# Performance work log

Measured on AMD Instinct MI355X. Metric: run time of the kernel, lower is better.

The kernel has to match this reference:

```python
import jax, jax.numpy as jnp
import numpy as np

N_NODES = 50000
IN, H, OUT = 128, 256, 128  # in_channels, hidden_channels, out_channels
E, PE = 640000, 500000
EPS = 1e-5


def setup_inputs() -> dict:
    key = jax.random.key(0)
    ks = jax.random.split(key, 12)
    def rn(k, shape, s=0.05):
        return jax.random.normal(k, shape, jnp.float32) * s
    return {
        "x": jax.random.normal(ks[0], (N_NODES, IN), jnp.float32),
        "edge_index": jax.random.randint(ks[1], (2, E), 0, N_NODES, jnp.int32),
        "pred_edge_index": jax.random.randint(ks[2], (2, PE), 0, N_NODES, jnp.int32),
        # SAGEConv 1: out = mean_neighbors @ W_l^T + x @ W_r^T + b (PyG default, root_weight=True)
        "W1l": rn(ks[3], (H, IN)), "W1r": rn(ks[4], (H, IN)), "b1": jnp.zeros((H,), jnp.float32),
        "bn1_g": jnp.ones((H,), jnp.float32), "bn1_b": jnp.zeros((H,), jnp.float32),
        "bn1_m": jnp.zeros((H,), jnp.float32), "bn1_v": jnp.ones((H,), jnp.float32),
        # SAGEConv 2
        "W2l": rn(ks[5], (OUT, H)), "W2r": rn(ks[6], (OUT, H)), "b2": jnp.zeros((OUT,), jnp.float32),
        # LinkPredictor MLP
        "pW1": rn(ks[7], (H, 2 * OUT)), "pb1": jnp.zeros((H,), jnp.float32),
        "pbn1_g": jnp.ones((H,), jnp.float32), "pbn1_b": jnp.zeros((H,), jnp.float32),
        "pbn1_m": jnp.zeros((H,), jnp.float32), "pbn1_v": jnp.ones((H,), jnp.float32),
        "pW2": rn(ks[8], (H // 2, H)), "pb2": jnp.zeros((H // 2,), jnp.float32),
        "pbn2_g": jnp.ones((H // 2,), jnp.float32), "pbn2_b": jnp.zeros((H // 2,), jnp.float32),
        "pbn2_m": jnp.zeros((H // 2,), jnp.float32), "pbn2_v": jnp.ones((H // 2,), jnp.float32),
        "pW3": rn(ks[9], (1, H // 2)), "pb3": jnp.zeros((1,), jnp.float32),
    }


def _bn(x, g, b, m, v):
    # BatchNorm1d in eval mode (running stats)
    return (x - m) * jax.lax.rsqrt(v + EPS) * g + b


def _sage(x, src, dst, Wl, Wr, b):
    # mean aggregation of source features onto targets (gather-scatter)
    agg = jax.ops.segment_sum(x[src], dst, num_segments=N_NODES)
    cnt = jax.ops.segment_sum(jnp.ones(src.shape, x.dtype), dst, num_segments=N_NODES)
    mean = agg / jnp.maximum(cnt, 1.0)[:, None]
    return mean @ Wl.T + x @ Wr.T + b


def reference(x, edge_index, pred_edge_index, W1l, W1r, b1, bn1_g, bn1_b, bn1_m, bn1_v,
              W2l, W2r, b2, pW1, pb1, pbn1_g, pbn1_b, pbn1_m, pbn1_v,
              pW2, pb2, pbn2_g, pbn2_b, pbn2_m, pbn2_v, pW3, pb3):
    src, dst = edge_index[0], edge_index[1]
    # encoder (dropout is identity in eval mode)
    h = _sage(x, src, dst, W1l, W1r, b1)
    h = jax.nn.relu(_bn(h, bn1_g, bn1_b, bn1_m, bn1_v))
    z = _sage(h, src, dst, W2l, W2r, b2)  # [N_NODES, OUT]
    # decoder: gather endpoint embeddings and run MLP
    q = jnp.concatenate([z[pred_edge_index[0]], z[pred_edge_index[1]]], axis=-1)  # [PE, 2*OUT]
    q = jax.nn.relu(_bn(q @ pW1.T + pb1, pbn1_g, pbn1_b, pbn1_m, pbn1_v))
    q = jax.nn.relu(_bn(q @ pW2.T + pb2, pbn2_g, pbn2_b, pbn2_m, pbn2_v))
    return (q @ pW3.T + pb3).squeeze(-1)  # [PE]
```

## Files before the change

### kernel.cpp

```cpp
#include <hip/hip_runtime.h>
#include <hip/hip_bf16.h>

#define NN   50000
#define NE   640000
#define NPE  500000
#define FEPS 1e-5f

typedef __attribute__((ext_vector_type(8))) short          bf16x8;
typedef __attribute__((ext_vector_type(8))) unsigned short u16x8;
typedef __attribute__((ext_vector_type(4))) float          f32x4;

__device__ inline float b2f(unsigned short u) {
    union { unsigned int i; float f; } c; c.i = (unsigned int)u << 16; return c.f;
}
__device__ inline unsigned short f2b(float f) {
    __hip_bfloat16 h = __float2bfloat16(f);
    return *reinterpret_cast<unsigned short*>(&h);
}

__global__ __launch_bounds__(256) void k_init(
    int4* __restrict__ zdst,
    const float* __restrict__ x, unsigned short* __restrict__ xbf,
    const float* __restrict__ W1l, const float* __restrict__ W1r,
    const float* __restrict__ W2l, const float* __restrict__ W2r,
    const float* __restrict__ pW1, const float* __restrict__ pW2,
    unsigned short* __restrict__ wdst) {
    int b = blockIdx.x, t = threadIdx.x;
    if (b < 98) {
        int i = b * 256 + t;
        if (i < 25088) zdst[i] = make_int4(0, 0, 0, 0);
        return;
    }
    const float* src;
    size_t off;
    if (b < 3223) {
        int i = (b - 98) * 256 + t;
        if (i >= 800000) return;
        const float4* p = (const float4*)x + 2 * (size_t)i;
        float4 a = p[0], c = p[1];
        u16x8 o;
        o[0]=f2b(a.x); o[1]=f2b(a.y); o[2]=f2b(a.z); o[3]=f2b(a.w);
        o[4]=f2b(c.x); o[5]=f2b(c.y); o[6]=f2b(c.z); o[7]=f2b(c.w);
        *((u16x8*)xbf + i) = o;
        return;
    }
    int i = (b - 3223) * 256 + t;
    if (i >= 28672) return;
    if      (i < 4096)  { src = W1l; off = i; }
    else if (i < 8192)  { src = W1r; off = i - 4096; }
    else if (i < 12288) { src = W2l; off = i - 8192; }
    else if (i < 16384) { src = W2r; off = i - 12288; }
    else if (i < 24576) { src = pW1; off = i - 16384; }
    else                { src = pW2; off = i - 24576; }
    const float4* p = (const float4*)src + 2 * off;
    float4 a = p[0], c = p[1];
    u16x8 o;
    o[0]=f2b(a.x); o[1]=f2b(a.y); o[2]=f2b(a.z); o[3]=f2b(a.w);
    o[4]=f2b(c.x); o[5]=f2b(c.y); o[6]=f2b(c.z); o[7]=f2b(c.w);
    *((u16x8*)wdst + i) = o;
}

__global__ void k_hist(const int* __restrict__ key, int* __restrict__ cnt, int n) {
    int e = blockIdx.x * blockDim.x + threadIdx.x;
    if (e < n) atomicAdd(&cnt[key[e]], 1);
}

__global__ void k_scan1(const int* __restrict__ cnt, int* __restrict__ part) {
    int t = threadIdx.x, lane = t & 63, w = t >> 6;
    int i = blockIdx.x * 256 + t;
    int v = (i < NN) ? cnt[i] : 0;
#pragma unroll
    for (int d = 1; d < 64; d <<= 1) v += __shfl_xor(v, d, 64);
    __shared__ int ws[4];
    if (lane == 0) ws[w] = v;
    __syncthreads();
    if (t == 0) part[blockIdx.x] = ws[0] + ws[1] + ws[2] + ws[3];
}

__global__ void k_scan2(int* __restrict__ part) {
    int t = threadIdx.x, lane = t & 63, w = t >> 6;
    int v = (t < 196) ? part[t] : 0;
    int s = v;
#pragma unroll
    for (int d = 1; d < 64; d <<= 1) { int u = __shfl_up(s, d, 64); if (lane >= d) s += u; }
    __shared__ int ws[4];
    if (lane == 63) ws[w] = s;
    __syncthreads();
    if (t == 0) { int a = 0; for (int k = 0; k < 4; ++k) { int tmp = ws[k]; ws[k] = a; a += tmp; } }
    __syncthreads();
    if (t < 196) part[t] = ws[w] + s - v;
}

__global__ void k_scan3(const int* __restrict__ cnt, const int* __restrict__ part,
                        int* __restrict__ rowptr) {
    int t = threadIdx.x, lane = t & 63, w = t >> 6;
    int i = blockIdx.x * 256 + t;
    int v = (i < NN) ? cnt[i] : 0;
    int s = v;
#pragma unroll
    for (int d = 1; d < 64; d <<= 1) { int u = __shfl_up(s, d, 64); if (lane >= d) s += u; }
    __shared__ int ws[4];
    if (lane == 63) ws[w] = s;
    __syncthreads();
    if (t == 0) { int a = 0; for (int k = 0; k < 4; ++k) { int tmp = ws[k]; ws[k] = a; a += tmp; } }
    __syncthreads();
    if (i <= NN) rowptr[i] = part[blockIdx.x] + ws[w] + s - v;
}

__global__ void k_fill(const int* __restrict__ src, const int* __restrict__ dst,
                       const int* __restrict__ rowptr, int* __restrict__ cursor,
                       int* __restrict__ col) {
    int e = blockIdx.x * blockDim.x + threadIdx.x;
    if (e >= NE) return;
    int d = dst[e];
    int slot = atomicAdd(&cursor[d], 1);
    col[rowptr[d] + slot] = src[e];
}

__global__ __launch_bounds__(256) void k_mean(const unsigned short* __restrict__ feat,
                                              const int* __restrict__ rowptr,
                                              const int* __restrict__ col,
                                              unsigned short* __restrict__ outm) {
    int node = blockIdx.x * 4 + (threadIdx.x >> 6);
    int lane = threadIdx.x & 63;
    int g = lane >> 4, li = lane & 15;
    if (node >= NN) return;
    int beg = rowptr[node], end = rowptr[node + 1];
    float acc[8];
#pragma unroll
    for (int k = 0; k < 8; ++k) acc[k] = 0.f;
    int j = beg;
    for (; j + 8 <= end; j += 8) {
        int s0 = col[j + g], s1 = col[j + 4 + g];
        u16x8 v0 = *(const u16x8*)(feat + (size_t)s0 * 128 + li * 8);
        u16x8 v1 = *(const u16x8*)(feat + (size_t)s1 * 128 + li * 8);
#pragma unroll
        for (int k = 0; k < 8; ++k)
            acc[k] += b2f((unsigned short)v0[k]) + b2f((unsigned short)v1[k]);
    }
    for (; j < end; j += 4) {
        int idx = j + g;
        bool ok = idx < end;
        int s = ok ? col[idx] : col[beg];
        u16x8 v = *(const u16x8*)(feat + (size_t)s * 128 + li * 8);
        if (ok) {
#pragma unroll
            for (int k = 0; k < 8; ++k) acc[k] += b2f((unsigned short)v[k]);
        }
    }
#pragma unroll
    for (int k = 0; k < 8; ++k) {
        acc[k] += __shfl_xor(acc[k], 16, 64);
        acc[k] += __shfl_xor(acc[k], 32, 64);
    }
    if (g == 0) {
        float inv = 1.f / fmaxf((float)(end - beg), 1.f);
        u16x8 o;
#pragma unroll
        for (int k = 0; k < 8; ++k) o[k] = f2b(acc[k] * inv);
        *(u16x8*)(outm + (size_t)node * 128 + li * 8) = o;
    }
}

__global__ __launch_bounds__(256) void k_sage12(
    const unsigned short* __restrict__ mean, const unsigned short* __restrict__ self,
    const unsigned short* __restrict__ Wl, const unsigned short* __restrict__ Wr,
    const float* __restrict__ b, const float* __restrict__ bg, const float* __restrict__ bb,
    const float* __restrict__ bm, const float* __restrict__ bv,
    const unsigned short* __restrict__ W2l, const unsigned short* __restrict__ W2r,
    const float* __restrict__ b2,
    unsigned short* __restrict__ Y, unsigned short* __restrict__ S) {
    __shared__ unsigned short AB[64 * 256];
    unsigned short* ms = AB;
    unsigned short* xs = AB + 64 * 128;
    int t = threadIdx.x;
    int n0 = blockIdx.x * 64;
    for (int j = 0; j < 4; ++j) {
        int idx = t + j * 256;
        int row = idx >> 4, c16 = idx & 15;
        int node = n0 + row;
        u16x8 v = {0,0,0,0,0,0,0,0}, v2 = {0,0,0,0,0,0,0,0};
        if (node < NN) {
            v  = *(const u16x8*)(mean + (size_t)node * 128 + c16 * 8);
            v2 = *(const u16x8*)(self + (size_t)node * 128 + c16 * 8);
        }
        int byte = row * 256 + ((c16 * 16) ^ ((row & 7) << 4));
        *(u16x8*)((char*)ms + byte) = v;
        *(u16x8*)((char*)xs + byte) = v2;
    }
    __syncthreads();
    int w = t >> 6, l = t & 63, lr = l & 15, lh = l >> 4;
    f32x4 acc[4][4];
#pragma unroll
    for (int mi = 0; mi < 4; ++mi)
#pragma unroll
        for (int ni = 0; ni < 4; ++ni) { acc[mi][ni][0]=0; acc[mi][ni][1]=0; acc[mi][ni][2]=0; acc[mi][ni][3]=0; }
#pragma unroll
    for (int half = 0; half < 2; ++half) {
        const unsigned short* A = half ? xs : ms;
        const unsigned short* W = half ? Wr : Wl;
#pragma unroll
        for (int ks = 0; ks < 4; ++ks) {
            int k0 = ks * 32;
            bf16x8 a[4], wf[4];
#pragma unroll
            for (int mi = 0; mi < 4; ++mi) {
                int row = mi * 16 + lr;
                int byte = row * 256 + ((k0 * 2 + lh * 16) ^ ((row & 7) << 4));
                a[mi] = *(const bf16x8*)((const char*)A + byte);
            }
#pragma unroll
            for (int ni = 0; ni < 4; ++ni) {
                int wrow = w * 64 + ni * 16 + lr;
                wf[ni] = *(const bf16x8*)(W + (size_t)wrow * 128 + k0 + lh * 8);
            }
#pragma unroll
            for (int mi = 0; mi < 4; ++mi)
#pragma unroll
                for (int ni = 0; ni < 4; ++ni)
                    acc[mi][ni] = __builtin_amdgcn_mfma_f32_16x16x32_bf16(a[mi], wf[ni], acc[mi][ni], 0, 0, 0);
        }
    }
    __syncthreads();
#pragma unroll
    for (int ni = 0; ni < 4; ++ni) {
        int ch = w * 64 + ni * 16 + lr;
        float sc = bg[ch] * rsqrtf(bv[ch] + FEPS);
        float sh = bb[ch] - bm[ch] * sc;
        float bias = b[ch];
#pragma unroll
        for (int mi = 0; mi < 4; ++mi)
#pragma unroll
            for (int r = 0; r < 4; ++r) {
                int row = mi * 16 + lh * 4 + r;
                float vv = fmaxf((acc[mi][ni][r] + bias) * sc + sh, 0.f);
                int byte = row * 512 + ((ch * 2) ^ ((row & 7) << 4));
                *(unsigned short*)((char*)AB + byte) = f2b(vv);
            }
    }
    __syncthreads();
    f32x4 aY[4][2], aS[4][2];
#pragma unroll
    for (int mi = 0; mi < 4; ++mi)
#pragma unroll
        for (int ni = 0; ni < 2; ++ni) {
            aY[mi][ni][0]=0; aY[mi][ni][1]=0; aY[mi][ni][2]=0; aY[mi][ni][3]=0;
            aS[mi][ni][0]=0; aS[mi][ni][1]=0; aS[mi][ni][2]=0; aS[mi][ni][3]=0;
        }
#pragma unroll
    for (int ks = 0; ks < 8; ++ks) {
        int k0 = ks * 32;
        bf16x8 a[4], wl[2], wr[2];
#pragma unroll
        for (int mi = 0; mi < 4; ++mi) {
            int row = mi * 16 + lr;
            int byte = row * 512 + ((k0 * 2 + lh * 16) ^ ((row & 7) << 4));
            a[mi] = *(const bf16x8*)((const char*)AB + byte);
        }
#pragma unroll
        for (int ni = 0; ni < 2; ++ni) {
            int wrow = w * 32 + ni * 16 + lr;
            wl[ni] = *(const bf16x8*)(W2l + (size_t)wrow * 256 + k0 + lh * 8);
            wr[ni] = *(const bf16x8*)(W2r + (size_t)wrow * 256 + k0 + lh * 8);
        }
#pragma unroll
        for (int mi = 0; mi < 4; ++mi)
#pragma unroll
            for (int ni = 0; ni < 2; ++ni) {
                aY[mi][ni] = __builtin_amdgcn_mfma_f32_16x16x32_bf16(a[mi], wl[ni], aY[mi][ni], 0, 0, 0);
                aS[mi][ni] = __builtin_amdgcn_mfma_f32_16x16x32_bf16(a[mi], wr[ni], aS[mi][ni], 0, 0, 0);
            }
    }
#pragma unroll
    for (int ni = 0; ni < 2; ++ni) {
        int ch = w * 32 + ni * 16 + lr;
        float bias = b2[ch];
#pragma unroll
        for (int mi = 0; mi < 4; ++mi)
#pragma unroll
            for (int r = 0; r < 4; ++r) {
                int node = n0 + mi * 16 + lh * 4 + r;
                if (node < NN) {
                    Y[(size_t)node * 128 + ch] = f2b(aY[mi][ni][r]);
                    S[(size_t)node * 128 + ch] = f2b(aS[mi][ni][r] + bias);
                }
            }
    }
}

__global__ __launch_bounds__(256) void k_prep(
    const unsigned short* __restrict__ S,
    const unsigned short* __restrict__ mY,
    const unsigned short* __restrict__ W1,
    const float* __restrict__ b1, const float* __restrict__ g1,
    const float* __restrict__ be1, const float* __restrict__ m1, const float* __restrict__ v1,
    unsigned short* __restrict__ Pa, unsigned short* __restrict__ Pb) {
    __shared__ unsigned short zs[64 * 128];
    int t = threadIdx.x;
    int n0 = blockIdx.x * 64;
    for (int j = 0; j < 4; ++j) {
        int idx = t + j * 256;
        int row = idx >> 4, c16 = idx & 15;
        int node = n0 + row;
        u16x8 o = {0,0,0,0,0,0,0,0};
        if (node < NN) {
            u16x8 sv = *(const u16x8*)(S  + (size_t)node * 128 + c16 * 8);
            u16x8 mv = *(const u16x8*)(mY + (size_t)node * 128 + c16 * 8);
#pragma unroll
            for (int jj = 0; jj < 8; ++jj)
                o[jj] = f2b(b2f((unsigned short)sv[jj]) + b2f((unsigned short)mv[jj]));
        }
        int byte = row * 256 + ((c16 * 16) ^ ((row & 7) << 4));
        *(u16x8*)((char*)zs + byte) = o;
    }
    __syncthreads();
    int w = t >> 6, l = t & 63, lr = l & 15, lh = l >> 4;
#pragma unroll
    for (int side = 0; side < 2; ++side) {
        f32x4 acc[4][4];
#pragma unroll
        for (int mi = 0; mi < 4; ++mi)
#pragma unroll
            for (int ni = 0; ni < 4; ++ni) { acc[mi][ni][0]=0; acc[mi][ni][1]=0; acc[mi][ni][2]=0; acc[mi][ni][3]=0; }
#pragma unroll
        for (int ks = 0; ks < 4; ++ks) {
            int k0 = ks * 32;
            bf16x8 a[4], wf[4];
#pragma unroll
            for (int mi = 0; mi < 4; ++mi) {
                int row = mi * 16 + lr;
                int byte = row * 256 + ((k0 * 2 + lh * 16) ^ ((row & 7) << 4));
                a[mi] = *(const bf16x8*)((const char*)zs + byte);
            }
#pragma unroll
            for (int ni = 0; ni < 4; ++ni) {
                int ch = w * 64 + ni * 16 + lr;
                wf[ni] = *(const bf16x8*)(W1 + (size_t)ch * 256 + side * 128 + k0 + lh * 8);
            }
#pragma unroll
            for (int mi = 0; mi < 4; ++mi)
#pragma unroll
                for (int ni = 0; ni < 4; ++ni)
                    acc[mi][ni] = __builtin_amdgcn_mfma_f32_16x16x32_bf16(a[mi], wf[ni], acc[mi][ni], 0, 0, 0);
        }
        unsigned short* P = side ? Pb : Pa;
#pragma unroll
        for (int ni = 0; ni < 4; ++ni) {
            int ch = w * 64 + ni * 16 + lr;
            float sc = g1[ch] * rsqrtf(v1[ch] + FEPS);
            float add = side ? 0.f : ((b1[ch] - m1[ch]) * sc + be1[ch]);
#pragma unroll
            for (int mi = 0; mi < 4; ++mi)
#pragma unroll
                for (int r = 0; r < 4; ++r) {
                    int node = n0 + mi * 16 + lh * 4 + r;
                    if (node < NN)
                        P[(size_t)node * 256 + ch] = f2b(acc[mi][ni][r] * sc + add);
                }
        }
    }
}

__global__ __launch_bounds__(256, 5) void k_mlp(
    const unsigned short* __restrict__ Pa, const unsigned short* __restrict__ Pb,
    const int* __restrict__ pu, const int* __restrict__ pv,
    const unsigned short* __restrict__ W2, const float* __restrict__ b2,
    const float* __restrict__ g2, const float* __restrict__ be2,
    const float* __restrict__ m2, const float* __restrict__ v2,
    const float* __restrict__ W3, const float* __restrict__ b3,
    float* __restrict__ out) {
    __shared__ unsigned short q1[64 * 256];
    int t = threadIdx.x;
    int e0 = blockIdx.x * 64;
#pragma unroll
    for (int batch = 0; batch < 2; ++batch) {
        u16x8 A[4], B[4];
        int bofs[4];
#pragma unroll
        for (int j = 0; j < 4; ++j) {
            int idx = t + (batch * 4 + j) * 256;
            int edge = idx >> 5, c16 = idx & 31;
            int ge = e0 + edge;
            if (ge < NPE) {
                int u = pu[ge], vv = pv[ge];
                A[j] = *(const u16x8*)(Pa + (size_t)u  * 256 + c16 * 8);
                B[j] = *(const u16x8*)(Pb + (size_t)vv * 256 + c16 * 8);
            } else {
                A[j] = (u16x8){0,0,0,0,0,0,0,0};
                B[j] = (u16x8){0,0,0,0,0,0,0,0};
            }
            bofs[j] = edge * 512 + ((c16 * 16) ^ ((edge & 7) << 4));
        }
#pragma unroll
        for (int j = 0; j < 4; ++j) {
            u16x8 o;
#pragma unroll
            for (int jj = 0; jj < 8; ++jj)
                o[jj] = f2b(fmaxf(b2f((unsigned short)A[j][jj]) + b2f((unsigned short)B[j][jj]), 0.f));
            *(u16x8*)((char*)q1 + bofs[j]) = o;
        }
    }
    __syncthreads();
    int w = t >> 6, l = t & 63, lr = l & 15, lh = l >> 4;
    f32x4 acc[4][2];
#pragma unroll
    for (int mi = 0; mi < 4; ++mi)
#pragma unroll
        for (int ni = 0; ni < 2; ++ni) { acc[mi][ni][0]=0; acc[mi][ni][1]=0; acc[mi][ni][2]=0; acc[mi][ni][3]=0; }
#pragma unroll
    for (int ks = 0; ks < 8; ++ks) {
        int k0 = ks * 32;
        bf16x8 a[4], wf[2];
#pragma unroll
        for (int mi = 0; mi < 4; ++mi) {
            int row = mi * 16 + lr;
            int byte = row * 512 + ((k0 * 2 + lh * 16) ^ ((row & 7) << 4));
            a[mi] = *(const bf16x8*)((const char*)q1 + byte);
        }
#pragma unroll
        for (int ni = 0; ni < 2; ++ni) {
            int wrow = w * 32 + ni * 16 + lr;
            wf[ni] = *(const bf16x8*)(W2 + (size_t)wrow * 256 + k0 + lh * 8);
        }
#pragma unroll
        for (int mi = 0; mi < 4; ++mi)
#pragma unroll
            for (int ni = 0; ni < 2; ++ni)
                acc[mi][ni] = __builtin_amdgcn_mfma_f32_16x16x32_bf16(a[mi], wf[ni], acc[mi][ni], 0, 0, 0);
    }
    __syncthreads();
#pragma unroll
    for (int ni = 0; ni < 2; ++ni) {
        int ch = w * 32 + ni * 16 + lr;
        float sc = g2[ch] * rsqrtf(v2[ch] + FEPS);
        float sh = be2[ch] - m2[ch] * sc;
        float bias = b2[ch];
#pragma unroll
        for (int mi = 0; mi < 4; ++mi)
#pragma unroll
            for (int r = 0; r < 4; ++r) {
                int row = mi * 16 + lh * 4 + r;
                float vv = fmaxf((acc[mi][ni][r] + bias) * sc + sh, 0.f);
                int byte = row * 256 + ((ch * 2) ^ ((row & 7) << 4));
                *(unsigned short*)((char*)q1 + byte) = f2b(vv);
            }
    }
    __syncthreads();
    {
        int edge = t >> 2, part = t & 3;
        float p = 0.f;
#pragma unroll
        for (int s = 0; s < 4; ++s) {
            int byte = edge * 256 + ((part * 64 + s * 16) ^ ((edge & 7) << 4));
            u16x8 v = *(const u16x8*)((const char*)q1 + byte);
#pragma unroll
            for (int jj = 0; jj < 8; ++jj)
                p += b2f((unsigned short)v[jj]) * W3[part * 32 + s * 8 + jj];
        }
        p += __shfl_xor(p, 1, 64);
        p += __shfl_xor(p, 2, 64);
        int ge = e0 + edge;
        if (part == 0 && ge < NPE) out[ge] = p + b3[0];
    }
}

extern "C" void kernel_launch(void* const* d_in, const int* in_sizes, int n_in,
                              void* d_out, int out_size, void* d_ws, size_t ws_size,
                              hipStream_t stream) {
    const float* x    = (const float*)d_in[0];
    const int*   ei   = (const int*)d_in[1];
    const int*   pei  = (const int*)d_in[2];
    const float* W1l  = (const float*)d_in[3];
    const float* W1r  = (const float*)d_in[4];
    const float* b1   = (const float*)d_in[5];
    const float* bn1g = (const float*)d_in[6];
    const float* bn1b = (const float*)d_in[7];
    const float* bn1m = (const float*)d_in[8];
    const float* bn1v = (const float*)d_in[9];
    const float* W2l  = (const float*)d_in[10];
    const float* W2r  = (const float*)d_in[11];
    const float* b2   = (const float*)d_in[12];
    const float* pW1  = (const float*)d_in[13];
    const float* pb1  = (const float*)d_in[14];
    const float* pg1  = (const float*)d_in[15];
    const float* pbb1 = (const float*)d_in[16];
    const float* pm1  = (const float*)d_in[17];
    const float* pv1  = (const float*)d_in[18];
    const float* pW2  = (const float*)d_in[19];
    const float* pb2  = (const float*)d_in[20];
    const float* pg2  = (const float*)d_in[21];
    const float* pbb2 = (const float*)d_in[22];
    const float* pm2  = (const float*)d_in[23];
    const float* pv2  = (const float*)d_in[24];
    const float* pW3  = (const float*)d_in[25];
    const float* pb3  = (const float*)d_in[26];
    float* out = (float*)d_out;

    const int* src = ei;
    const int* dst = ei + NE;
    const int* pu  = pei;
    const int* pv  = pei + NPE;

    char* p = (char*)d_ws;
    auto alloc = [&](size_t bytes) -> char* {
        char* r = p; p += (bytes + 255) & ~(size_t)255; return r;
    };
    int* cnt     = (int*)alloc((size_t)NN * 4);
    int* cursor  = (int*)alloc((size_t)NN * 4);
    int* part    = (int*)alloc(256 * 4);
    int* rowptr  = (int*)alloc((size_t)(NN + 1) * 4);
    int* col     = (int*)alloc((size_t)NE * 4);
    unsigned short* xbf  = (unsigned short*)alloc((size_t)NN * 128 * 2);
    unsigned short* mx   = (unsigned short*)alloc((size_t)NN * 128 * 2);
    unsigned short* Ybf  = (unsigned short*)alloc((size_t)NN * 128 * 2);
    unsigned short* mY   = (unsigned short*)alloc((size_t)NN * 128 * 2);
    unsigned short* Sbf  = (unsigned short*)alloc((size_t)NN * 128 * 2);
    unsigned short* Pa   = (unsigned short*)alloc((size_t)NN * 256 * 2);
    unsigned short* W1lb = (unsigned short*)alloc((size_t)256 * 128 * 2);
    unsigned short* W1rb = (unsigned short*)alloc((size_t)256 * 128 * 2);
    unsigned short* W2lb = (unsigned short*)alloc((size_t)128 * 256 * 2);
    unsigned short* W2rb = (unsigned short*)alloc((size_t)128 * 256 * 2);
    unsigned short* pW1b = (unsigned short*)alloc((size_t)256 * 256 * 2);
    unsigned short* pW2b = (unsigned short*)alloc((size_t)128 * 256 * 2);
    unsigned short* Pb = xbf;

    k_init<<<3335, 256, 0, stream>>>((int4*)cnt, x, xbf,
                                     W1l, W1r, W2l, W2r, pW1, pW2, W1lb);
    k_hist<<<2500, 256, 0, stream>>>(dst, cnt, NE);
    k_scan1<<<196, 256, 0, stream>>>(cnt, part);
    k_scan2<<<1, 256, 0, stream>>>(part);
    k_scan3<<<196, 256, 0, stream>>>(cnt, part, rowptr);
    k_fill<<<2500, 256, 0, stream>>>(src, dst, rowptr, cursor, col);

    k_mean<<<12500, 256, 0, stream>>>(xbf, rowptr, col, mx);
    k_sage12<<<782, 256, 0, stream>>>(mx, xbf, W1lb, W1rb, b1, bn1g, bn1b, bn1m, bn1v,
                                      W2lb, W2rb, b2, Ybf, Sbf);
    k_mean<<<12500, 256, 0, stream>>>(Ybf, rowptr, col, mY);

    k_prep<<<782, 256, 0, stream>>>(Sbf, mY, pW1b, pb1, pg1, pbb1, pm1, pv1, Pa, Pb);

    k_mlp<<<(NPE + 63) / 64, 256, 0, stream>>>(Pa, Pb, pu, pv,
                                               pW2b, pb2, pg2, pbb2, pm2, pv2,
                                               pW3, pb3, out);
}
```

Before: 346.8 us.

## Prefetch second edge tile during MLP compute and fold scan2 into scan3

k_mlp now handles two 64-edge tiles per block. The gathers for the second tile are issued into registers while the first tile's MFMA and epilogue run, which is meant to hide the random-access gather latency behind compute. This raises register pressure, so occupancy is lowered from 5 to 4 blocks per SIMD, and the grid is halved. Separately, the single-block scan2 launch is removed: each scan3 block now reduces the block partials before it directly, saving one launch at the cost of some redundant reads.

Result: slower. 400.0 us (+15.4%).

```diff
diff --git a/kernel.cpp b/kernel.cpp
--- a/kernel.cpp
+++ b/kernel.cpp
@@ -77,34 +77,28 @@
     if (t == 0) part[blockIdx.x] = ws[0] + ws[1] + ws[2] + ws[3];
 }
 
-__global__ void k_scan2(int* __restrict__ part) {
-    int t = threadIdx.x, lane = t & 63, w = t >> 6;
-    int v = (t < 196) ? part[t] : 0;
-    int s = v;
-#pragma unroll
-    for (int d = 1; d < 64; d <<= 1) { int u = __shfl_up(s, d, 64); if (lane >= d) s += u; }
-    __shared__ int ws[4];
-    if (lane == 63) ws[w] = s;
-    __syncthreads();
-    if (t == 0) { int a = 0; for (int k = 0; k < 4; ++k) { int tmp = ws[k]; ws[k] = a; a += tmp; } }
-    __syncthreads();
-    if (t < 196) part[t] = ws[w] + s - v;
-}
-
 __global__ void k_scan3(const int* __restrict__ cnt, const int* __restrict__ part,
                         int* __restrict__ rowptr) {
     int t = threadIdx.x, lane = t & 63, w = t >> 6;
+    __shared__ int ws[4];
+    __shared__ int sbase;
+    int pvv = (t < 196 && t < blockIdx.x) ? part[t] : 0;
+#pragma unroll
+    for (int d = 1; d < 64; d <<= 1) pvv += __shfl_xor(pvv, d, 64);
+    if (lane == 0) ws[w] = pvv;
+    __syncthreads();
+    if (t == 0) sbase = ws[0] + ws[1] + ws[2] + ws[3];
+    __syncthreads();
     int i = blockIdx.x * 256 + t;
     int v = (i < NN) ? cnt[i] : 0;
     int s = v;
 #pragma unroll
     for (int d = 1; d < 64; d <<= 1) { int u = __shfl_up(s, d, 64); if (lane >= d) s += u; }
-    __shared__ int ws[4];
     if (lane == 63) ws[w] = s;
     __syncthreads();
     if (t == 0) { int a = 0; for (int k = 0; k < 4; ++k) { int tmp = ws[k]; ws[k] = a; a += tmp; } }
     __syncthreads();
-    if (i <= NN) rowptr[i] = part[blockIdx.x] + ws[w] + s - v;
+    if (i <= NN) rowptr[i] = sbase + ws[w] + s - v;
 }
 
 __global__ void k_fill(const int* __restrict__ src, const int* __restrict__ dst,
@@ -361,7 +355,7 @@
     }
 }
 
-__global__ __launch_bounds__(256, 5) void k_mlp(
+__global__ __launch_bounds__(256, 4) void k_mlp(
     const unsigned short* __restrict__ Pa, const unsigned short* __restrict__ Pb,
     const int* __restrict__ pu, const int* __restrict__ pv,
     const unsigned short* __restrict__ W2, const float* __restrict__ b2,
@@ -371,7 +365,10 @@
     float* __restrict__ out) {
     __shared__ unsigned short q1[64 * 256];
     int t = threadIdx.x;
-    int e0 = blockIdx.x * 64;
+    int w = t >> 6, l = t & 63, lr = l & 15, lh = l >> 4;
+    int e0 = blockIdx.x * 128;
+    int e1 = e0 + 64;
+
 #pragma unroll
     for (int batch = 0; batch < 2; ++batch) {
         u16x8 A[4], B[4];
@@ -400,8 +397,25 @@
             *(u16x8*)((char*)q1 + bofs[j]) = o;
         }
     }
-    __syncthreads();
-    int w = t >> 6, l = t & 63, lr = l & 15, lh = l >> 4;
+    u16x8 A1a[4], B1a[4];
+    int bofs1a[4];
+#pragma unroll
+    for (int j = 0; j < 4; ++j) {
+        int idx = t + j * 256;
+        int edge = idx >> 5, c16 = idx & 31;
+        int ge = e1 + edge;
+        if (ge < NPE) {
+            int u = pu[ge], vv = pv[ge];
+            A1a[j] = *(const u16x8*)(Pa + (size_t)u  * 256 + c16 * 8);
+            B1a[j] = *(const u16x8*)(Pb + (size_t)vv * 256 + c16 * 8);
+        } else {
+            A1a[j] = (u16x8){0,0,0,0,0,0,0,0};
+            B1a[j] = (u16x8){0,0,0,0,0,0,0,0};
+        }
+        bofs1a[j] = edge * 512 + ((c16 * 16) ^ ((edge & 7) << 4));
+    }
+    __syncthreads();
+
     f32x4 acc[4][2];
 #pragma unroll
     for (int mi = 0; mi < 4; ++mi)
@@ -428,7 +442,25 @@
             for (int ni = 0; ni < 2; ++ni)
                 acc[mi][ni] = __builtin_amdgcn_mfma_f32_16x16x32_bf16(a[mi], wf[ni], acc[mi][ni], 0, 0, 0);
     }
-    __syncthreads();
+    u16x8 A1b[4], B1b[4];
+    int bofs1b[4];
+#pragma unroll
+    for (int j = 0; j < 4; ++j) {
+        int idx = t + (4 + j) * 256;
+        int edge = idx >> 5, c16 = idx & 31;
+        int ge = e1 + edge;
+        if (ge < NPE) {
+            int u = pu[ge], vv = pv[ge];
+            A1b[j] = *(const u16x8*)(Pa + (size_t)u  * 256 + c16 * 8);
+            B1b[j] = *(const u16x8*)(Pb + (size_t)vv * 256 + c16 * 8);
+        } else {
+            A1b[j] = (u16x8){0,0,0,0,0,0,0,0};
+            B1b[j] = (u16x8){0,0,0,0,0,0,0,0};
+        }
+        bofs1b[j] = edge * 512 + ((c16 * 16) ^ ((edge & 7) << 4));
+    }
+    __syncthreads();
+
 #pragma unroll
     for (int ni = 0; ni < 2; ++ni) {
         int ch = w * 32 + ni * 16 + lr;
@@ -460,6 +492,85 @@
         p += __shfl_xor(p, 1, 64);
         p += __shfl_xor(p, 2, 64);
         int ge = e0 + edge;
+        if (part == 0 && ge < NPE) out[ge] = p + b3[0];
+    }
+    __syncthreads();
+
+#pragma unroll
+    for (int j = 0; j < 4; ++j) {
+        u16x8 o;
+#pragma unroll
+        for (int jj = 0; jj < 8; ++jj)
+            o[jj] = f2b(fmaxf(b2f((unsigned short)A1a[j][jj]) + b2f((unsigned short)B1a[j][jj]), 0.f));
+        *(u16x8*)((char*)q1 + bofs1a[j]) = o;
+    }
+#pragma unroll
+    for (int j = 0; j < 4; ++j) {
+        u16x8 o;
+#pragma unroll
+        for (int jj = 0; jj < 8; ++jj)
+            o[jj] = f2b(fmaxf(b2f((unsigned short)A1b[j][jj]) + b2f((unsigned short)B1b[j][jj]), 0.f));
+        *(u16x8*)((char*)q1 + bofs1b[j]) = o;
+    }
+    __syncthreads();
+
+#pragma unroll
+    for (int mi = 0; mi < 4; ++mi)
+#pragma unroll
+        for (int ni = 0; ni < 2; ++ni) { acc[mi][ni][0]=0; acc[mi][ni][1]=0; acc[mi][ni][2]=0; acc[mi][ni][3]=0; }
+#pragma unroll
+    for (int ks = 0; ks < 8; ++ks) {
+        int k0 = ks * 32;
+        bf16x8 a[4], wf[2];
+#pragma unroll
+        for (int mi = 0; mi < 4; ++mi) {
+            int row = mi * 16 + lr;
+            int byte = row * 512 + ((k0 * 2 + lh * 16) ^ ((row & 7) << 4));
+            a[mi] = *(const bf16x8*)((const char*)q1 + byte);
+        }
+#pragma unroll
+        for (int ni = 0; ni < 2; ++ni) {
+            int wrow = w * 32 + ni * 16 + lr;
+            wf[ni] = *(const bf16x8*)(W2 + (size_t)wrow * 256 + k0 + lh * 8);
+        }
+#pragma unroll
+        for (int mi = 0; mi < 4; ++mi)
+#pragma unroll
+            for (int ni = 0; ni < 2; ++ni)
+                acc[mi][ni] = __builtin_amdgcn_mfma_f32_16x16x32_bf16(a[mi], wf[ni], acc[mi][ni], 0, 0, 0);
+    }
+    __syncthreads();
+#pragma unroll
+    for (int ni = 0; ni < 2; ++ni) {
+        int ch = w * 32 + ni * 16 + lr;
+        float sc = g2[ch] * rsqrtf(v2[ch] + FEPS);
+        float sh = be2[ch] - m2[ch] * sc;
+        float bias = b2[ch];
+#pragma unroll
+        for (int mi = 0; mi < 4; ++mi)
+#pragma unroll
+            for (int r = 0; r < 4; ++r) {
+                int row = mi * 16 + lh * 4 + r;
+                float vv = fmaxf((acc[mi][ni][r] + bias) * sc + sh, 0.f);
+                int byte = row * 256 + ((ch * 2) ^ ((row & 7) << 4));
+                *(unsigned short*)((char*)q1 + byte) = f2b(vv);
+            }
+    }
+    __syncthreads();
+    {
+        int edge = t >> 2, part = t & 3;
+        float p = 0.f;
+#pragma unroll
+        for (int s = 0; s < 4; ++s) {
+            int byte = edge * 256 + ((part * 64 + s * 16) ^ ((edge & 7) << 4));
+            u16x8 v = *(const u16x8*)((const char*)q1 + byte);
+#pragma unroll
+            for (int jj = 0; jj < 8; ++jj)
+                p += b2f((unsigned short)v[jj]) * W3[part * 32 + s * 8 + jj];
+        }
+        p += __shfl_xor(p, 1, 64);
+        p += __shfl_xor(p, 2, 64);
+        int ge = e1 + edge;
         if (part == 0 && ge < NPE) out[ge] = p + b3[0];
     }
 }
@@ -528,7 +639,6 @@
                                      W1l, W1r, W2l, W2r, pW1, pW2, W1lb);
     k_hist<<<2500, 256, 0, stream>>>(dst, cnt, NE);
     k_scan1<<<196, 256, 0, stream>>>(cnt, part);
-    k_scan2<<<1, 256, 0, stream>>>(part);
     k_scan3<<<196, 256, 0, stream>>>(cnt, part, rowptr);
     k_fill<<<2500, 256, 0, stream>>>(src, dst, rowptr, cursor, col);
 
@@ -539,7 +649,7 @@
 
     k_prep<<<782, 256, 0, stream>>>(Sbf, mY, pW1b, pb1, pg1, pbb1, pm1, pv1, Pa, Pb);
 
-    k_mlp<<<(NPE + 63) / 64, 256, 0, stream>>>(Pa, Pb, pu, pv,
-                                               pW2b, pb2, pg2, pbb2, pm2, pv2,
-                                               pW3, pb3, out);
-}
+    k_mlp<<<(NPE + 127) / 128, 256, 0, stream>>>(Pa, Pb, pu, pv,
+                                                 pW2b, pb2, pg2, pbb2, pm2, pv2,
+                                                 pW3, pb3, out);
+}
```
